# Kernel optimization log

Measured on AMD Instinct MI355X. Metric: run time of the kernel, lower is better.

## Reference

```python
import jax, jax.numpy as jnp
import numpy as np

B, P, D = 8, 1024, 768
H = 12
HD = D // H


def setup_inputs() -> dict:
    key = jax.random.key(0)
    k1, k2, k3, k4, k5 = jax.random.split(key, 5)
    s = 0.02
    return {
        "x": jax.random.normal(k1, (B, P, D), dtype=jnp.float32),
        "w_qkv": jax.random.normal(k2, (D, 3 * D), dtype=jnp.float32) * s,
        "b_qkv": jax.random.normal(k3, (3 * D,), dtype=jnp.float32) * s,
        "w_proj": jax.random.normal(k4, (D, D), dtype=jnp.float32) * s,
        "b_proj": jax.random.normal(k5, (D,), dtype=jnp.float32) * s,
    }


def reference(x, w_qkv, b_qkv, w_proj, b_proj):
    b, p, d = x.shape
    scale = HD ** -0.5
    qkv = x @ w_qkv + b_qkv                      # [B,P,3D]
    qkv = qkv.reshape(b, p, 3, H, HD).transpose(2, 0, 3, 1, 4)  # [3,B,H,P,HD]
    q, k, v = qkv[0], qkv[1], qkv[2]
    attn = jnp.einsum("bhqd,bhkd->bhqk", q, k) * scale
    attn = jax.nn.softmax(attn, axis=-1)         # attn_drop is identity (p=0)
    weighted_avg = jnp.einsum("bhqk,bhkd->bhqd", attn, v)
    weighted_avg = weighted_avg.transpose(0, 2, 1, 3).reshape(b, p, d)  # [B,P,D]
    out = weighted_avg @ w_proj + b_proj         # proj_drop is identity (p=0)
    return (out, weighted_avg)
```

## Files before the change

### kernel.cpp

```cpp
#include <hip/hip_runtime.h>
#include <hip/hip_bf16.h>


typedef __attribute__((ext_vector_type(8))) short short8;
typedef __attribute__((ext_vector_type(4))) float f32x4;

#define MFMA_BF16(a, b, c) __builtin_amdgcn_mfma_f32_16x16x32_bf16((a), (b), (c), 0, 0, 0)

#define NB 8
#define NP 1024
#define ND 768
#define NH 12
#define NHD 64
#define NTOK (NB * NP)
#define N3D (3 * ND)
#define OUT_HALF (NTOK * ND)
#define QSCALE 0.18033688f

__device__ __forceinline__ void gload_lds16(const void* gptr, void* ldsptr) {
  __builtin_amdgcn_global_load_lds(
      (const __attribute__((address_space(1))) unsigned int*)gptr,
      (__attribute__((address_space(3))) unsigned int*)ldsptr, 16, 0, 0);
}

__device__ __forceinline__ unsigned pack_bf16x2(float a, float b) {
  __hip_bfloat162 h = __float22bfloat162_rn(float2{a, b});
  return *reinterpret_cast<unsigned*>(&h);
}


__global__ void k_cvt_x(const float* __restrict__ in, __hip_bfloat16* __restrict__ out) {
  int i = (blockIdx.x * 256 + threadIdx.x) * 8;
  float4 a = *(const float4*)(in + i);
  float4 b = *(const float4*)(in + i + 4);
  union { __hip_bfloat16 h[8]; uint4 u; } r;
  r.h[0] = __float2bfloat16(a.x); r.h[1] = __float2bfloat16(a.y);
  r.h[2] = __float2bfloat16(a.z); r.h[3] = __float2bfloat16(a.w);
  r.h[4] = __float2bfloat16(b.x); r.h[5] = __float2bfloat16(b.y);
  r.h[6] = __float2bfloat16(b.z); r.h[7] = __float2bfloat16(b.w);
  *(uint4*)(out + i) = r.u;
}

__global__ void k_cvt_t(const float* __restrict__ in, __hip_bfloat16* __restrict__ out,
                        int K, int N) {
  __shared__ float tile[32][33];
  int k0 = blockIdx.x * 32;
  int n0 = blockIdx.y * 32;
  int r = threadIdx.x >> 5;
  int c = threadIdx.x & 31;
#pragma unroll
  for (int i = 0; i < 4; ++i)
    tile[r + 8 * i][c] = in[(size_t)(k0 + r + 8 * i) * N + n0 + c];
  __syncthreads();
#pragma unroll
  for (int i = 0; i < 4; ++i)
    out[(size_t)(n0 + r + 8 * i) * K + k0 + c] = __float2bfloat16(tile[c][r + 8 * i]);
}


__device__ __forceinline__ void gemm_mainloop(const __hip_bfloat16* __restrict__ A,
                                              const __hip_bfloat16* __restrict__ BT,
                                              int m0, int n0, char* Ls,
                                              f32x4 acc[4][4]) {
  const int tid = threadIdx.x;
  const int wid = tid >> 6, lane = tid & 63;
  const int wm = wid >> 1, wn = wid & 1;
  const int lrow = lane & 15, lk = lane >> 4;
  constexpr int K = 768, NKT = K / 32;

#define STAGE_G(kt, bi)                                                  \
  {                                                                      \
    const int k0s = (kt) * 32;                                           \
    char* dst = Ls + (bi) * 16384;                                       \
    _Pragma("unroll")                                                    \
    for (int t = 0; t < 2; ++t) {                                        \
      int o = (tid + t * 256) * 16;        \
      int mr = o >> 6;                    \
      int kk = (o & 63) >> 1;                   \
      gload_lds16(A + (size_t)(m0 + mr) * K + k0s + kk,                  \
                  dst + wid * 1024 + t * 4096);                          \
      gload_lds16(BT + (size_t)(n0 + mr) * K + k0s + kk,                 \
                  dst + 8192 + wid * 1024 + t * 4096);                   \
    }                                                                    \
  }

#define COMPUTE_T(kt)                                                          \
  {                                                                            \
    const char* buf = Ls + ((kt) % 3) * 16384;                                 \
    short8 af[4], bf[4];                                                       \
    _Pragma("unroll")                                                          \
    for (int i = 0; i < 4; ++i) {                                              \
      af[i] = *(const short8*)(buf + (wm * 64 + i * 16 + lrow) * 64 + lk * 16);\
      bf[i] = *(const short8*)(buf + 8192 +                                    \
                               (wn * 64 + i * 16 + lrow) * 64 + lk * 16);      \
    }                                                                          \
    _Pragma("unroll")                                                          \
    for (int mi = 0; mi < 4; ++mi)                                             \
      _Pragma("unroll")                                                        \
      for (int ni = 0; ni < 4; ++ni)                                           \
        acc[mi][ni] = MFMA_BF16(af[mi], bf[ni], acc[mi][ni]);                  \
  }

  STAGE_G(0, 0);
  STAGE_G(1, 1);

#pragma unroll 3
  for (int kt = 0; kt < NKT - 1; ++kt) {
    asm volatile("s_waitcnt vmcnt(4)" ::: "memory");
    __builtin_amdgcn_s_barrier();
    if (kt + 2 < NKT) STAGE_G(kt + 2, (kt + 2) % 3);
    COMPUTE_T(kt);
  }
  asm volatile("s_waitcnt vmcnt(0)" ::: "memory");
  __builtin_amdgcn_s_barrier();
  COMPUTE_T(NKT - 1);

#undef STAGE_G
#undef COMPUTE_T
}


__launch_bounds__(256)
__global__ void k_qkv_gemm(const __hip_bfloat16* __restrict__ A,
                           const __hip_bfloat16* __restrict__ BT,
                           const float* __restrict__ bias,
                           __hip_bfloat16* __restrict__ q_ws,
                           __hip_bfloat16* __restrict__ k_ws,
                           __hip_bfloat16* __restrict__ v_ws) {
  __shared__ char Ls[3 * 16384];
  const int mt = blockIdx.x & 63, nt = blockIdx.x >> 6;
  const int m0 = mt * 128, n0 = nt * 128;
  const int wid = threadIdx.x >> 6, lane = threadIdx.x & 63;
  const int wm = wid >> 1, wn = wid & 1;
  const int lrow = lane & 15, lk = lane >> 4;

  f32x4 acc[4][4] = {};
  gemm_mainloop(A, BT, m0, n0, Ls, acc);

  const int which = n0 / ND;
#pragma unroll
  for (int ni = 0; ni < 4; ++ni) {
    const int n = n0 + wn * 64 + ni * 16 + lrow;
    const float bv = bias[n];
    const int hh = (n % ND) >> 6;
    const int hd = n & 63;
#pragma unroll
    for (int mi = 0; mi < 4; ++mi) {
      const int mbase = m0 + wm * 64 + mi * 16 + lk * 4;
#pragma unroll
      for (int i = 0; i < 4; ++i) {
        const int m = mbase + i;
        const float v = acc[mi][ni][i] + bv;
        const int b = m >> 10, p = m & 1023;
        const int bh = b * NH + hh;
        if (which == 0)      q_ws[((size_t)bh * NP + p) * NHD + hd] = __float2bfloat16(v * QSCALE);
        else if (which == 1) k_ws[((size_t)bh * NP + p) * NHD + hd] = __float2bfloat16(v);
        else                 v_ws[((size_t)bh * NHD + hd) * NP + p] = __float2bfloat16(v);
      }
    }
  }
}


#define KVBLK 64

__launch_bounds__(256)
__global__ void k_attn(const __hip_bfloat16* __restrict__ q_ws,
                       const __hip_bfloat16* __restrict__ k_ws,
                       const __hip_bfloat16* __restrict__ v_ws,
                       float* __restrict__ wavg_f32,
                       __hip_bfloat16* __restrict__ wavg_bf) {
  __shared__ char smem[2 * 16384 + 4 * 2304];
  const int bh = blockIdx.y;
  const int tid = threadIdx.x;
  const int wid = tid >> 6, lane = tid & 63;
  const int lrow = lane & 15, lk = lane >> 4;
  const int q0 = blockIdx.x * 64 + wid * 16;
  char* pbuf = smem + 32768 + wid * 2304;

  const __hip_bfloat16* Qb = q_ws + (size_t)bh * NP * NHD;
  const __hip_bfloat16* Kb = k_ws + (size_t)bh * NP * NHD;
  const __hip_bfloat16* Vb = v_ws + (size_t)bh * NHD * NP;

  short8 qf0 = *(const short8*)(Qb + (size_t)(q0 + lrow) * NHD + lk * 8);
  short8 qf1 = *(const short8*)(Qb + (size_t)(q0 + lrow) * NHD + 32 + lk * 8);

  f32x4 acc[4] = {};
  float dsa = 0.f, dsb = 0.f;

#define STAGE(buf, key0)                                                          \
  {                                                                               \
    _Pragma("unroll")                                                             \
    for (int p = 0; p < 2; ++p) {                                                 \
      const int L = p * 4096 + tid * 16;                                          \
      const int r = L >> 7;                                                       \
      const int cb = L & 127;                                                     \
      const int sc = (cb ^ ((r & 7) << 4)) >> 1;        \
      gload_lds16(Kb + (size_t)((key0) + r) * NHD + sc, (buf) + L);               \
      gload_lds16(Vb + (size_t)r * NP + (key0) + sc, (buf) + 8192 + L);           \
    }                                                                             \
  }

  char* cur = smem;
  char* nxt = smem + 16384;
  STAGE(cur, 0);
  __syncthreads();

  for (int kc = 0; kc < NP / KVBLK; ++kc) {
    if (kc < NP / KVBLK - 1) STAGE(nxt, (kc + 1) * KVBLK);

    char* Ks = cur;
    char* Vs = cur + 8192;

    f32x4 s[4];
#pragma unroll
    for (int kt = 0; kt < 4; ++kt) {
      const int row = kt * 16 + lrow;
      const int sw = (row & 7) << 4;
      short8 klo = *(const short8*)(Ks + row * 128 + ((lk * 16) ^ sw));
      short8 khi = *(const short8*)(Ks + row * 128 + ((64 + lk * 16) ^ sw));
      f32x4 z = {0.f, 0.f, 0.f, 0.f};
      s[kt] = MFMA_BF16(klo, qf0, z);
      s[kt] = MFMA_BF16(khi, qf1, s[kt]);
    }

#pragma unroll
    for (int kt = 0; kt < 4; ++kt) {
      const float p0 = __builtin_amdgcn_exp2f(s[kt][0]);
      const float p1 = __builtin_amdgcn_exp2f(s[kt][1]);
      const float p2 = __builtin_amdgcn_exp2f(s[kt][2]);
      const float p3 = __builtin_amdgcn_exp2f(s[kt][3]);
      dsa += p0 + p1;
      dsb += p2 + p3;
      uint2 w;
      w.x = pack_bf16x2(p0, p1);
      w.y = pack_bf16x2(p2, p3);
      *(uint2*)(pbuf + lrow * 144 + kt * 32 + lk * 8) = w;
    }

#pragma unroll
    for (int kh = 0; kh < 2; ++kh) {
      short8 a2 = *(const short8*)(pbuf + lrow * 144 + kh * 64 + lk * 16);
#pragma unroll
      for (int hdt = 0; hdt < 4; ++hdt) {
        const int row = hdt * 16 + lrow;
        short8 vf = *(const short8*)(Vs + row * 128 +
                                     ((kh * 64 + lk * 16) ^ ((row & 7) << 4)));
        acc[hdt] = MFMA_BF16(a2, vf, acc[hdt]);
      }
    }

    __syncthreads();
    char* t = cur; cur = nxt; nxt = t;
  }

  float ds = dsa + dsb;
  ds += __shfl_xor(ds, 16);
  ds += __shfl_xor(ds, 32);
  float rd[4];
#pragma unroll
  for (int i = 0; i < 4; ++i) rd[i] = 1.0f / __shfl(ds, lk * 4 + i, 16);

  const int b = bh / NH, hh = bh % NH;
#pragma unroll
  for (int hdt = 0; hdt < 4; ++hdt) {
#pragma unroll
    for (int i = 0; i < 4; ++i) {
      const int qq = q0 + lk * 4 + i;
      const int col = hh * NHD + hdt * 16 + lrow;
      const float val = acc[hdt][i] * rd[i];
      const size_t o = ((size_t)b * NP + qq) * ND + col;
      wavg_f32[o] = val;
      wavg_bf[o] = __float2bfloat16(val);
    }
  }
#undef STAGE
}


__launch_bounds__(256)
__global__ void k_proj_gemm(const __hip_bfloat16* __restrict__ A,
                            const __hip_bfloat16* __restrict__ BT,
                            const float* __restrict__ bias,
                            float* __restrict__ C) {
  __shared__ char Ls[3 * 16384];
  const int mt = blockIdx.x & 63, nt = blockIdx.x >> 6;
  const int m0 = mt * 128, n0 = nt * 128;
  const int wid = threadIdx.x >> 6, lane = threadIdx.x & 63;
  const int wm = wid >> 1, wn = wid & 1;
  const int lrow = lane & 15, lk = lane >> 4;

  f32x4 acc[4][4] = {};
  gemm_mainloop(A, BT, m0, n0, Ls, acc);

#pragma unroll
  for (int ni = 0; ni < 4; ++ni) {
    const int n = n0 + wn * 64 + ni * 16 + lrow;
    const float bv = bias[n];
#pragma unroll
    for (int mi = 0; mi < 4; ++mi) {
      const int mbase = m0 + wm * 64 + mi * 16 + lk * 4;
#pragma unroll
      for (int i = 0; i < 4; ++i)
        C[(size_t)(mbase + i) * ND + n] = acc[mi][ni][i] + bv;
    }
  }
}


extern "C" void kernel_launch(void* const* d_in, const int* in_sizes, int n_in,
                              void* d_out, int out_size, void* d_ws, size_t ws_size,
                              hipStream_t stream) {
  const float* x      = (const float*)d_in[0];
  const float* w_qkv  = (const float*)d_in[1];
  const float* b_qkv  = (const float*)d_in[2];
  const float* w_proj = (const float*)d_in[3];
  const float* b_proj = (const float*)d_in[4];
  float* out = (float*)d_out;
  float* wavg_out = out + OUT_HALF;

  char* ws = (char*)d_ws;
  __hip_bfloat16* xbf    = (__hip_bfloat16*)(ws);
  __hip_bfloat16* wqkvT  = (__hip_bfloat16*)(ws + 12582912);
  __hip_bfloat16* wprojT = (__hip_bfloat16*)(ws + 16121856);
  __hip_bfloat16* q_ws   = (__hip_bfloat16*)(ws + 17301504);
  __hip_bfloat16* k_ws   = (__hip_bfloat16*)(ws + 29884416);
  __hip_bfloat16* v_ws   = (__hip_bfloat16*)(ws + 42467328);
  __hip_bfloat16* wavg_bf = xbf;

  k_cvt_x<<<NTOK * ND / (256 * 8), 256, 0, stream>>>(x, xbf);
  k_cvt_t<<<dim3(ND / 32, N3D / 32), 256, 0, stream>>>(w_qkv, wqkvT, ND, N3D);
  k_cvt_t<<<dim3(ND / 32, ND / 32), 256, 0, stream>>>(w_proj, wprojT, ND, ND);
  k_qkv_gemm<<<(NTOK / 128) * (N3D / 128), 256, 0, stream>>>(xbf, wqkvT, b_qkv,
                                                             q_ws, k_ws, v_ws);
  k_attn<<<dim3(NP / 64, NB * NH), 256, 0, stream>>>(q_ws, k_ws, v_ws, wavg_out, wavg_bf);
  k_proj_gemm<<<(NTOK / 128) * (ND / 128), 256, 0, stream>>>(wavg_bf, wprojT, b_proj, out);
}
```

Baseline: 134.2 us.

## Widen GEMM tiles to 128x256 with LDS swizzle, XCD remap, and MFMA priority

Both GEMMs now use 128x256 tiles, with each wave owning a full 128x64 strip (8x4 MFMA accumulators). The A and B LDS tiles are XOR-swizzled to cut bank conflicts, and block indices are remapped across the 8 XCDs for cache locality. Launch bounds request two blocks per CU. The attention kernel also raises wave priority around its MFMA sections. The larger tiles are meant to improve operand reuse and cut LDS traffic, but they double accumulator registers and grow LDS to 72KB per block, which may lower occupancy.

```diff
diff --git a/kernel.cpp b/kernel.cpp
--- a/kernel.cpp
+++ b/kernel.cpp
@@ -27,6 +27,8 @@
   __hip_bfloat162 h = __float22bfloat162_rn(float2{a, b});
   return *reinterpret_cast<unsigned*>(&h);
 }
+
+__device__ __forceinline__ int swz_g(int b) { return b ^ (((b >> 7) & 7) << 4); }
 
 
 __global__ void k_cvt_x(const float* __restrict__ in, __hip_bfloat16* __restrict__ out) {
@@ -61,44 +63,54 @@
 __device__ __forceinline__ void gemm_mainloop(const __hip_bfloat16* __restrict__ A,
                                               const __hip_bfloat16* __restrict__ BT,
                                               int m0, int n0, char* Ls,
-                                              f32x4 acc[4][4]) {
+                                              f32x4 acc[8][4]) {
   const int tid = threadIdx.x;
   const int wid = tid >> 6, lane = tid & 63;
-  const int wm = wid >> 1, wn = wid & 1;
   const int lrow = lane & 15, lk = lane >> 4;
   constexpr int K = 768, NKT = K / 32;
 
-#define STAGE_G(kt, bi)                                                  \
-  {                                                                      \
-    const int k0s = (kt) * 32;                                           \
-    char* dst = Ls + (bi) * 16384;                                       \
-    _Pragma("unroll")                                                    \
-    for (int t = 0; t < 2; ++t) {                                        \
-      int o = (tid + t * 256) * 16;        \
-      int mr = o >> 6;                    \
-      int kk = (o & 63) >> 1;                   \
-      gload_lds16(A + (size_t)(m0 + mr) * K + k0s + kk,                  \
-                  dst + wid * 1024 + t * 4096);                          \
-      gload_lds16(BT + (size_t)(n0 + mr) * K + k0s + kk,                 \
-                  dst + 8192 + wid * 1024 + t * 4096);                   \
-    }                                                                    \
-  }
-
-#define COMPUTE_T(kt)                                                          \
-  {                                                                            \
-    const char* buf = Ls + ((kt) % 3) * 16384;                                 \
-    short8 af[4], bf[4];                                                       \
-    _Pragma("unroll")                                                          \
-    for (int i = 0; i < 4; ++i) {                                              \
-      af[i] = *(const short8*)(buf + (wm * 64 + i * 16 + lrow) * 64 + lk * 16);\
-      bf[i] = *(const short8*)(buf + 8192 +                                    \
-                               (wn * 64 + i * 16 + lrow) * 64 + lk * 16);      \
-    }                                                                          \
-    _Pragma("unroll")                                                          \
-    for (int mi = 0; mi < 4; ++mi)                                             \
-      _Pragma("unroll")                                                        \
-      for (int ni = 0; ni < 4; ++ni)                                           \
-        acc[mi][ni] = MFMA_BF16(af[mi], bf[ni], acc[mi][ni]);                  \
+  int aoff[8], boff[4];
+#pragma unroll
+  for (int i = 0; i < 8; ++i)
+    aoff[i] = swz_g((i * 16 + lrow) * 64 + lk * 16);
+#pragma unroll
+  for (int j = 0; j < 4; ++j)
+    boff[j] = swz_g((wid * 64 + j * 16 + lrow) * 64 + lk * 16);
+
+#define STAGE_G(kt, bi)                                                     \
+  {                                                                         \
+    const int k0s = (kt) * 32;                                              \
+    char* dst = Ls + (bi) * 24576;                                          \
+    _Pragma("unroll")                                                       \
+    for (int t = 0; t < 2; ++t) {                              \
+      const int L = t * 4096 + tid * 16;                                    \
+      const int lb = swz_g(L);                                              \
+      gload_lds16(A + (size_t)(m0 + (lb >> 6)) * K + k0s + ((lb & 63) >> 1),\
+                  dst + L);                                                 \
+    }                                                                       \
+    _Pragma("unroll")                                                       \
+    for (int t = 0; t < 4; ++t) {                             \
+      const int L = t * 4096 + tid * 16;                                    \
+      const int lb = swz_g(L);                                              \
+      gload_lds16(BT + (size_t)(n0 + (lb >> 6)) * K + k0s + ((lb & 63) >> 1),\
+                  dst + 8192 + L);                                          \
+    }                                                                       \
+  }
+
+#define COMPUTE_T(kt)                                                       \
+  {                                                                         \
+    const char* buf = Ls + ((kt) % 3) * 24576;                              \
+    short8 bfr[4];                                                          \
+    _Pragma("unroll")                                                       \
+    for (int j = 0; j < 4; ++j)                                             \
+      bfr[j] = *(const short8*)(buf + 8192 + boff[j]);                      \
+    _Pragma("unroll")                                                       \
+    for (int i = 0; i < 8; ++i) {                                           \
+      short8 afr = *(const short8*)(buf + aoff[i]);                         \
+      _Pragma("unroll")                                                     \
+      for (int j = 0; j < 4; ++j)                                           \
+        acc[i][j] = MFMA_BF16(afr, bfr[j], acc[i][j]);                      \
+    }                                                                       \
   }
 
   STAGE_G(0, 0);
@@ -106,7 +118,7 @@
 
 #pragma unroll 3
   for (int kt = 0; kt < NKT - 1; ++kt) {
-    asm volatile("s_waitcnt vmcnt(4)" ::: "memory");
+    asm volatile("s_waitcnt vmcnt(6)" ::: "memory");
     __builtin_amdgcn_s_barrier();
     if (kt + 2 < NKT) STAGE_G(kt + 2, (kt + 2) % 3);
     COMPUTE_T(kt);
@@ -120,37 +132,37 @@
 }
 
 
-__launch_bounds__(256)
+__launch_bounds__(256, 2)
 __global__ void k_qkv_gemm(const __hip_bfloat16* __restrict__ A,
                            const __hip_bfloat16* __restrict__ BT,
                            const float* __restrict__ bias,
                            __hip_bfloat16* __restrict__ q_ws,
                            __hip_bfloat16* __restrict__ k_ws,
                            __hip_bfloat16* __restrict__ v_ws) {
-  __shared__ char Ls[3 * 16384];
-  const int mt = blockIdx.x & 63, nt = blockIdx.x >> 6;
-  const int m0 = mt * 128, n0 = nt * 128;
+  __shared__ char Ls[3 * 24576];
+  const int wg = (blockIdx.x & 7) * 72 + (blockIdx.x >> 3);
+  const int mt = wg & 63, nt = wg >> 6;
+  const int m0 = mt * 128, n0 = nt * 256;
   const int wid = threadIdx.x >> 6, lane = threadIdx.x & 63;
-  const int wm = wid >> 1, wn = wid & 1;
   const int lrow = lane & 15, lk = lane >> 4;
 
-  f32x4 acc[4][4] = {};
+  f32x4 acc[8][4] = {};
   gemm_mainloop(A, BT, m0, n0, Ls, acc);
 
   const int which = n0 / ND;
 #pragma unroll
-  for (int ni = 0; ni < 4; ++ni) {
-    const int n = n0 + wn * 64 + ni * 16 + lrow;
+  for (int j = 0; j < 4; ++j) {
+    const int n = n0 + wid * 64 + j * 16 + lrow;
     const float bv = bias[n];
     const int hh = (n % ND) >> 6;
     const int hd = n & 63;
 #pragma unroll
-    for (int mi = 0; mi < 4; ++mi) {
-      const int mbase = m0 + wm * 64 + mi * 16 + lk * 4;
-#pragma unroll
-      for (int i = 0; i < 4; ++i) {
-        const int m = mbase + i;
-        const float v = acc[mi][ni][i] + bv;
+    for (int i = 0; i < 8; ++i) {
+      const int mbase = m0 + i * 16 + lk * 4;
+#pragma unroll
+      for (int r = 0; r < 4; ++r) {
+        const int m = mbase + r;
+        const float v = acc[i][j][r] + bv;
         const int b = m >> 10, p = m & 1023;
         const int bh = b * NH + hh;
         if (which == 0)      q_ws[((size_t)bh * NP + p) * NHD + hd] = __float2bfloat16(v * QSCALE);
@@ -213,6 +225,7 @@
     char* Vs = cur + 8192;
 
     f32x4 s[4];
+    __builtin_amdgcn_s_setprio(1);
 #pragma unroll
     for (int kt = 0; kt < 4; ++kt) {
       const int row = kt * 16 + lrow;
@@ -223,6 +236,7 @@
       s[kt] = MFMA_BF16(klo, qf0, z);
       s[kt] = MFMA_BF16(khi, qf1, s[kt]);
     }
+    __builtin_amdgcn_s_setprio(0);
 
 #pragma unroll
     for (int kt = 0; kt < 4; ++kt) {
@@ -238,6 +252,7 @@
       *(uint2*)(pbuf + lrow * 144 + kt * 32 + lk * 8) = w;
     }
 
+    __builtin_amdgcn_s_setprio(1);
 #pragma unroll
     for (int kh = 0; kh < 2; ++kh) {
       short8 a2 = *(const short8*)(pbuf + lrow * 144 + kh * 64 + lk * 16);
@@ -249,6 +264,7 @@
         acc[hdt] = MFMA_BF16(a2, vf, acc[hdt]);
       }
     }
+    __builtin_amdgcn_s_setprio(0);
 
     __syncthreads();
     char* t = cur; cur = nxt; nxt = t;
@@ -278,31 +294,31 @@
 }
 
 
-__launch_bounds__(256)
+__launch_bounds__(256, 2)
 __global__ void k_proj_gemm(const __hip_bfloat16* __restrict__ A,
                             const __hip_bfloat16* __restrict__ BT,
                             const float* __restrict__ bias,
                             float* __restrict__ C) {
-  __shared__ char Ls[3 * 16384];
-  const int mt = blockIdx.x & 63, nt = blockIdx.x >> 6;
-  const int m0 = mt * 128, n0 = nt * 128;
+  __shared__ char Ls[3 * 24576];
+  const int wg = (blockIdx.x & 7) * 24 + (blockIdx.x >> 3);
+  const int mt = wg & 63, nt = wg >> 6;
+  const int m0 = mt * 128, n0 = nt * 256;
   const int wid = threadIdx.x >> 6, lane = threadIdx.x & 63;
-  const int wm = wid >> 1, wn = wid & 1;
   const int lrow = lane & 15, lk = lane >> 4;
 
-  f32x4 acc[4][4] = {};
+  f32x4 acc[8][4] = {};
   gemm_mainloop(A, BT, m0, n0, Ls, acc);
 
 #pragma unroll
-  for (int ni = 0; ni < 4; ++ni) {
-    const int n = n0 + wn * 64 + ni * 16 + lrow;
+  for (int j = 0; j < 4; ++j) {
+    const int n = n0 + wid * 64 + j * 16 + lrow;
     const float bv = bias[n];
 #pragma unroll
-    for (int mi = 0; mi < 4; ++mi) {
-      const int mbase = m0 + wm * 64 + mi * 16 + lk * 4;
-#pragma unroll
-      for (int i = 0; i < 4; ++i)
-        C[(size_t)(mbase + i) * ND + n] = acc[mi][ni][i] + bv;
+    for (int i = 0; i < 8; ++i) {
+      const int mbase = m0 + i * 16 + lk * 4;
+#pragma unroll
+      for (int r = 0; r < 4; ++r)
+        C[(size_t)(mbase + r) * ND + n] = acc[i][j][r] + bv;
     }
   }
 }
@@ -331,8 +347,8 @@
   k_cvt_x<<<NTOK * ND / (256 * 8), 256, 0, stream>>>(x, xbf);
   k_cvt_t<<<dim3(ND / 32, N3D / 32), 256, 0, stream>>>(w_qkv, wqkvT, ND, N3D);
   k_cvt_t<<<dim3(ND / 32, ND / 32), 256, 0, stream>>>(w_proj, wprojT, ND, ND);
-  k_qkv_gemm<<<(NTOK / 128) * (N3D / 128), 256, 0, stream>>>(xbf, wqkvT, b_qkv,
+  k_qkv_gemm<<<(NTOK / 128) * (N3D / 256), 256, 0, stream>>>(xbf, wqkvT, b_qkv,
                                                              q_ws, k_ws, v_ws);
   k_attn<<<dim3(NP / 64, NB * NH), 256, 0, stream>>>(q_ws, k_ws, v_ws, wavg_out, wavg_bf);
-  k_proj_gemm<<<(NTOK / 128) * (ND / 128), 256, 0, stream>>>(wavg_bf, wprojT, b_proj, out);
-}
+  k_proj_gemm<<<(NTOK / 128) * (ND / 256), 256, 0, stream>>>(wavg_bf, wprojT, b_proj, out);
+}
```

Measured after the change: 159.9 us. 1.19x slower.
